# Optimization experiments

Measured on AMD Instinct MI355X. Metric: run time of the kernel, lower is better.

## Reference

```python
import jax, jax.numpy as jnp
import numpy as np

B, N, E1, H, D = 16, 256, 4, 8, 128  # batch, max nodes, edge types+1, heads, dim
VOCAB = 100


def setup_inputs() -> dict:
    key = jax.random.key(0)
    ks = jax.random.split(key, 20)
    s = 0.05
    return dict(
        node_feat=jax.random.randint(ks[0], (B, N), 0, VOCAB),
        L=jax.random.normal(ks[1], (B, N, N, E1), jnp.float32),
        emb=jax.random.normal(ks[2], (VOCAB, D), jnp.float32) * s,
        W0=jax.random.normal(ks[3], (E1, H, D, D), jnp.float32) * s,
        W1=jax.random.normal(ks[4], (E1, H, D * H * E1, D), jnp.float32) * (s / 4.0),
        a1w0=jax.random.normal(ks[5], (E1, H, D), jnp.float32) * s,
        a1b0=jnp.zeros((E1, H), jnp.float32),
        a2w0=jax.random.normal(ks[6], (E1, H, D), jnp.float32) * s,
        a2b0=jnp.zeros((E1, H), jnp.float32),
        a1w1=jax.random.normal(ks[7], (E1, H, D), jnp.float32) * s,
        a1b1=jnp.zeros((E1, H), jnp.float32),
        a2w1=jax.random.normal(ks[8], (E1, H, D), jnp.float32) * s,
        a2b1=jnp.zeros((E1, H), jnp.float32),
        sb0=jnp.zeros((E1, H, D), jnp.float32),
        sb1=jnp.zeros((E1, H, D), jnp.float32),
        outW=jax.random.normal(ks[9], (D, D), jnp.float32) * s,
        outb=jnp.zeros((D,), jnp.float32),
        attW=jax.random.normal(ks[10], (D,), jnp.float32) * s,
        attb=jnp.zeros((), jnp.float32),
    )


def _gat_layer(state, Ltr, W, a1w, a1b, a2w, a2b, sb, last):
    # state: (B, N, Din); W: (E1, H, Din, D); Ltr: (E1, 1, B, N, N)
    Wh = jnp.einsum('bni,ehio->ehbno', state, W)                      # (E1,H,B,N,D)
    s1 = jnp.einsum('ehbno,eho->ehbn', Wh, a1w) + a1b[:, :, None, None]
    s2 = jnp.einsum('ehbno,eho->ehbn', Wh, a2w) + a2b[:, :, None, None]
    logits = jax.nn.leaky_relu(s1[..., :, None] + s2[..., None, :], 0.2) + Ltr
    att = jax.nn.softmax(logits, axis=3)  # torch softmax over dim=1 of (B,N,N)
    h = jnp.einsum('ehbnm,ehbmo->ehbno', att, Wh) + sb[:, :, None, None, :]
    if last:
        return jnp.mean(h, axis=(0, 1))                               # (B,N,D)
    h = jax.nn.elu(h)
    # concat order in torch: outer edge-type jj, inner head ii -> (B,N,E1*H*D)
    return jnp.transpose(h, (2, 3, 0, 1, 4)).reshape(state.shape[0], state.shape[1], -1)


def reference(node_feat, L, emb, W0, W1, a1w0, a1b0, a2w0, a2b0,
              a1w1, a1b1, a2w1, a2b1, sb0, sb1, outW, outb, attW, attb):
    Ltr = jnp.transpose(L, (3, 0, 1, 2))[:, None]  # (E1,1,B,N,N)
    state = emb[node_feat]                         # (B,N,D)
    state = _gat_layer(state, Ltr, W0, a1w0, a1b0, a2w0, a2b0, sb0, last=False)
    state = _gat_layer(state, Ltr, W1, a1w1, a1b1, a2w1, a2b1, sb1, last=True)
    y = state @ outW + outb                        # (B,N,D)
    aw = jax.nn.sigmoid(state @ attW + attb)       # (B,N)
    y = aw[..., None] * y
    return jnp.mean(y, axis=1)                     # (B,D)
```

## Files before the change

kernel.cpp:

```cpp
#include <hip/hip_runtime.h>
#include <hip/hip_bf16.h>

#define Bq 16
#define Nq 256
#define E1q 4
#define Hq 8
#define Dq 128
#define EH 32
#define BN 4096

typedef __hip_bfloat16 bf16;
typedef short bf16x8 __attribute__((ext_vector_type(8)));
typedef float f32x4 __attribute__((ext_vector_type(4)));

__device__ __forceinline__ void gll16(const void* gptr, void* lptr) {
    __builtin_amdgcn_global_load_lds(
        (const __attribute__((address_space(1))) void*)gptr,
        (__attribute__((address_space(3))) void*)lptr, 16, 0, 0);
}

__device__ __forceinline__ unsigned short f2bf(float v) {
    __hip_bfloat16 h = __float2bfloat16(v);
    return *(unsigned short*)&h;
}

__device__ __forceinline__ void transpose_tile(const float* __restrict__ W,
                                               bf16* __restrict__ WT, int K,
                                               int kt, int nt, int eh,
                                               float (*tile)[65], int tid) {
    int tr = tid >> 6, tc = tid & 63;
    const float* src = W + ((size_t)eh * K + kt * 64) * 128 + nt * 64;
#pragma unroll
    for (int p = 0; p < 16; ++p) {
        int r = p * 4 + tr;
        tile[r][tc] = src[(size_t)r * 128 + tc];
    }
    __syncthreads();
    bf16* dst = WT + ((size_t)eh * 128 + nt * 64) * K + kt * 64;
    int cg = tid & 15, rs = tid >> 4;
#pragma unroll
    for (int p = 0; p < 4; ++p) {
        int n = rs + 16 * p;
        ushort4 pk;
        pk.x = f2bf(tile[cg * 4 + 0][n]);
        pk.y = f2bf(tile[cg * 4 + 1][n]);
        pk.z = f2bf(tile[cg * 4 + 2][n]);
        pk.w = f2bf(tile[cg * 4 + 3][n]);
        *(ushort4*)(dst + (size_t)n * K + cg * 4) = pk;
    }
}

__global__ __launch_bounds__(256) void prep_kernel(const int* __restrict__ nf,
                                                   const float* __restrict__ emb,
                                                   const float* __restrict__ W0,
                                                   const float* __restrict__ W1,
                                                   const float* __restrict__ L,
                                                   bf16* __restrict__ st0b,
                                                   bf16* __restrict__ W0T,
                                                   bf16* __restrict__ W1T,
                                                   float* __restrict__ Le) {
    int bid = blockIdx.x;
    int t = threadIdx.x;
    __shared__ float tile[64][65];
    if (bid < 2048) {
        int i = bid * 256 + t;
        int row = i >> 7, col = i & 127;
        st0b[i] = __float2bfloat16(emb[nf[row] * Dq + col]);
    } else if (bid < 2176) {
        int id2 = bid - 2048;
        transpose_tile(W0, W0T, 128, id2 & 1, (id2 >> 1) & 1, id2 >> 2, tile, t);
    } else if (bid < 6272) {
        int id3 = bid - 2176;
        transpose_tile(W1, W1T, 4096, id3 & 63, (id3 >> 6) & 1, id3 >> 7, tile, t);
    } else {
        int idx = (bid - 6272) * 256 + t;
        float4 v = *(const float4*)(L + (size_t)idx * 4);
        Le[idx] = v.x;
        Le[1048576 + idx] = v.y;
        Le[2097152 + idx] = v.z;
        Le[3145728 + idx] = v.w;
    }
}

__global__ __launch_bounds__(256) void mfma_gemm_kernel(const bf16* __restrict__ Ab,
                                                        const bf16* __restrict__ Bt,
                                                        bf16* __restrict__ Wht,
                                                        const float* __restrict__ a1w,
                                                        const float* __restrict__ a1b,
                                                        const float* __restrict__ a2w,
                                                        const float* __restrict__ a2b,
                                                        float* __restrict__ s1,
                                                        float* __restrict__ s2, int K) {
    int id = blockIdx.x;
    int xcd = id & 7, slot = id >> 3;
    int eh = (slot & 3) * 8 + xcd;
    int rt = slot >> 2;
    int tid = threadIdx.x;
    int w = tid >> 6, l = tid & 63;
    int q = l >> 4, mn = l & 15;
    __shared__ __align__(16) bf16 As[128 * 64];
    __shared__ __align__(16) bf16 Bs[128 * 64];
    __shared__ float red1[128], red2[128];
    const bf16* Ap = Ab + (size_t)(rt * 128) * K;
    const bf16* Bp = Bt + (size_t)eh * 128 * K;
    int lr = l >> 3;
    int g = (l & 7) ^ lr;
    int gcol = g * 8;

    if (tid < 128) { red1[tid] = 0.f; red2[tid] = 0.f; }

    f32x4 acc[4][4];
#pragma unroll
    for (int i = 0; i < 4; i++)
#pragma unroll
        for (int j = 0; j < 4; j++) acc[i][j] = (f32x4){0.f, 0.f, 0.f, 0.f};

    int wr = (w >> 1) * 64, wc = (w & 1) * 64;
    int msw = mn & 7;

    for (int k0 = 0; k0 < K; k0 += 64) {
#pragma unroll
        for (int u = 0; u < 4; ++u) {
            int i = w * 4 + u;
            int r = i * 8 + lr;
            gll16(Ap + (size_t)r * K + k0 + gcol, (char*)As + i * 1024);
            gll16(Bp + (size_t)r * K + k0 + gcol, (char*)Bs + i * 1024);
        }
        __syncthreads();
#pragma unroll
        for (int kk = 0; kk < 2; ++kk) {
            int qb = ((kk * 4 + q) ^ msw) * 16;
            bf16x8 af[4], bfr[4];
#pragma unroll
            for (int i = 0; i < 4; ++i) {
                af[i]  = *(const bf16x8*)((const char*)As + (wr + i * 16 + mn) * 128 + qb);
                bfr[i] = *(const bf16x8*)((const char*)Bs + (wc + i * 16 + mn) * 128 + qb);
            }
#pragma unroll
            for (int i = 0; i < 4; ++i)
#pragma unroll
                for (int j = 0; j < 4; ++j)
                    acc[i][j] = __builtin_amdgcn_mfma_f32_16x16x32_bf16(af[i], bfr[j], acc[i][j], 0, 0, 0);
        }
        __syncthreads();
    }
#pragma unroll
    for (int i = 0; i < 4; ++i) {
        int r0 = rt * 128 + wr + i * 16 + q * 4;
        int b = r0 >> 8, m = r0 & 255;
#pragma unroll
        for (int j = 0; j < 4; ++j) {
            int o = wc + j * 16 + mn;
            ushort4 pk;
            pk.x = f2bf(acc[i][j][0]);
            pk.y = f2bf(acc[i][j][1]);
            pk.z = f2bf(acc[i][j][2]);
            pk.w = f2bf(acc[i][j][3]);
            *(ushort4*)(Wht + ((((size_t)eh * 16 + b) * 128 + o) * 256 + m)) = pk;
        }
    }
    float w1v[4], w2v[4];
#pragma unroll
    for (int j = 0; j < 4; ++j) {
        int o = wc + j * 16 + mn;
        w1v[j] = a1w[eh * 128 + o];
        w2v[j] = a2w[eh * 128 + o];
    }
#pragma unroll
    for (int i = 0; i < 4; ++i)
#pragma unroll
        for (int r = 0; r < 4; ++r) {
            float p1 = 0.f, p2 = 0.f;
#pragma unroll
            for (int j = 0; j < 4; ++j) {
                p1 += acc[i][j][r] * w1v[j];
                p2 += acc[i][j][r] * w2v[j];
            }
#pragma unroll
            for (int off = 1; off < 16; off <<= 1) {
                p1 += __shfl_xor(p1, off);
                p2 += __shfl_xor(p2, off);
            }
            if (mn == 0) {
                int row = wr + i * 16 + q * 4 + r;
                atomicAdd(&red1[row], p1);
                atomicAdd(&red2[row], p2);
            }
        }
    __syncthreads();
    if (tid < 128) {
        int rg = rt * 128 + tid;
        s1[eh * 4096 + rg] = red1[tid] + a1b[eh];
        s2[eh * 4096 + rg] = red2[tid] + a2b[eh];
    }
}

__global__ __launch_bounds__(512, 2) void gemm4k_kernel(const bf16* __restrict__ Ab,
                                                        const bf16* __restrict__ Bt,
                                                        bf16* __restrict__ Wht,
                                                        const float* __restrict__ a1w,
                                                        const float* __restrict__ a1b,
                                                        const float* __restrict__ a2w,
                                                        const float* __restrict__ a2b,
                                                        float* __restrict__ s1,
                                                        float* __restrict__ s2) {
    __shared__ __align__(16) char smem[131072];
    int bid = blockIdx.x;
    int wg = (bid & 7) * 32 + (bid >> 3);
    int tm = wg >> 4, tn = wg & 15;
    int tid = threadIdx.x;
    int wid = tid >> 6, l = tid & 63;
    int wr = wid >> 2, wc = wid & 3;
    int lhi = l >> 4, llo = l & 15;
    int skq = (l & 7) ^ ((l >> 3) & 7);

    const bf16* Ap = Ab + (size_t)tm * 256 * 4096;
    const bf16* Bp = Bt + (size_t)tn * 256 * 4096;
    const bf16* sA = Ap + (size_t)(wid * 8 + (l >> 3)) * 4096 + skq * 8;
    const bf16* sB = Bp + (size_t)(wid * 8 + (l >> 3)) * 4096 + skq * 8;
    char* dA = (char*)smem + wid * 1024;
    char* dB = (char*)smem + 32768 + wid * 1024;

    auto stA = [&](int tt, int s) {
        gll16(sA + (size_t)s * 64 * 4096 + tt * 64, dA + (tt & 1) * 65536 + s * 8192);
    };
    auto stB = [&](int tt, int s) {
        gll16(sB + (size_t)s * 64 * 4096 + tt * 64, dB + (tt & 1) * 65536 + s * 8192);
    };

    f32x4 acc[8][4];
#pragma unroll
    for (int i = 0; i < 8; ++i)
#pragma unroll
        for (int j = 0; j < 4; ++j) acc[i][j] = (f32x4){0.f, 0.f, 0.f, 0.f};

    int kp0 = ((lhi)     ^ (llo & 7)) << 4;
    int kp1 = ((4 + lhi) ^ (llo & 7)) << 4;
    int aoff = (wr * 64 + llo) << 7;
    int boff = 32768 + ((wc * 32 + llo) << 7);

    stA(0, 0); stA(0, 1); stB(0, 0); stB(0, 1);
    stA(0, 2); stA(0, 3); stB(0, 2); stB(0, 3);
    asm volatile("s_waitcnt vmcnt(0)" ::: "memory");
    __builtin_amdgcn_s_barrier();
    bf16x8 A0[4][2], A1[4][2], B0[2][2], B1[2][2];
    {
        const char* sm0 = (const char*)smem;
#pragma unroll
        for (int m = 0; m < 4; ++m) {
            A0[m][0] = *(const bf16x8*)(sm0 + aoff + m * 2048 + kp0);
            A0[m][1] = *(const bf16x8*)(sm0 + aoff + m * 2048 + kp1);
        }
#pragma unroll
        for (int n = 0; n < 2; ++n) {
            B0[n][0] = *(const bf16x8*)(sm0 + boff + n * 2048 + kp0);
            B0[n][1] = *(const bf16x8*)(sm0 + boff + n * 2048 + kp1);
        }
    }

#pragma unroll 1
    for (int t = 0; t < 64; ++t) {
        const char* smc = (const char*)smem + (t & 1) * 65536;
        const char* smn = (const char*)smem + (((t + 1) & 1)) * 65536;
#pragma unroll
        for (int m = 0; m < 4; ++m) {
            A1[m][0] = *(const bf16x8*)(smc + aoff + 16384 + m * 2048 + kp0);
            A1[m][1] = *(const bf16x8*)(smc + aoff + 16384 + m * 2048 + kp1);
        }
        if (t < 63) { stA(t + 1, 0); stA(t + 1, 1); stB(t + 1, 0); stB(t + 1, 1); }
        asm volatile("s_waitcnt lgkmcnt(8)" ::: "memory");
        __builtin_amdgcn_sched_barrier(0);
        __builtin_amdgcn_s_setprio(1);
#pragma unroll
        for (int ks = 0; ks < 2; ++ks)
#pragma unroll
            for (int m = 0; m < 4; ++m)
#pragma unroll
                for (int n = 0; n < 2; ++n)
                    acc[m][n] = __builtin_amdgcn_mfma_f32_16x16x32_bf16(A0[m][ks], B0[n][ks], acc[m][n], 0, 0, 0);
        __builtin_amdgcn_s_setprio(0);
#pragma unroll
        for (int n = 0; n < 2; ++n) {
            B1[n][0] = *(const bf16x8*)(smc + boff + 16384 + n * 2048 + kp0);
            B1[n][1] = *(const bf16x8*)(smc + boff + 16384 + n * 2048 + kp1);
        }
        if (t < 63) { stA(t + 1, 2); stA(t + 1, 3); stB(t + 1, 2); stB(t + 1, 3); }
        asm volatile("s_waitcnt lgkmcnt(4)" ::: "memory");
        __builtin_amdgcn_sched_barrier(0);
        __builtin_amdgcn_s_setprio(1);
#pragma unroll
        for (int ks = 0; ks < 2; ++ks)
#pragma unroll
            for (int m = 0; m < 4; ++m)
#pragma unroll
                for (int n = 0; n < 2; ++n)
                    acc[4 + m][n] = __builtin_amdgcn_mfma_f32_16x16x32_bf16(A1[m][ks], B0[n][ks], acc[4 + m][n], 0, 0, 0);
        __builtin_amdgcn_s_setprio(0);
        asm volatile("s_waitcnt lgkmcnt(0)" ::: "memory");
        __builtin_amdgcn_sched_barrier(0);
        __builtin_amdgcn_s_setprio(1);
#pragma unroll
        for (int ks = 0; ks < 2; ++ks)
#pragma unroll
            for (int m = 0; m < 4; ++m)
#pragma unroll
                for (int n = 0; n < 2; ++n)
                    acc[m][2 + n] = __builtin_amdgcn_mfma_f32_16x16x32_bf16(A0[m][ks], B1[n][ks], acc[m][2 + n], 0, 0, 0);
        __builtin_amdgcn_s_setprio(0);
        if (t < 63) { asm volatile("s_waitcnt vmcnt(4)" ::: "memory"); }
        __builtin_amdgcn_s_barrier();
        if (t < 63) {
#pragma unroll
            for (int m = 0; m < 4; ++m) {
                A0[m][0] = *(const bf16x8*)(smn + aoff + m * 2048 + kp0);
                A0[m][1] = *(const bf16x8*)(smn + aoff + m * 2048 + kp1);
            }
#pragma unroll
            for (int n = 0; n < 2; ++n) {
                B0[n][0] = *(const bf16x8*)(smn + boff + n * 2048 + kp0);
                B0[n][1] = *(const bf16x8*)(smn + boff + n * 2048 + kp1);
            }
        }
        __builtin_amdgcn_sched_barrier(0);
        __builtin_amdgcn_s_setprio(1);
#pragma unroll
        for (int ks = 0; ks < 2; ++ks)
#pragma unroll
            for (int m = 0; m < 4; ++m)
#pragma unroll
                for (int n = 0; n < 2; ++n)
                    acc[4 + m][2 + n] = __builtin_amdgcn_mfma_f32_16x16x32_bf16(A1[m][ks], B1[n][ks], acc[4 + m][2 + n], 0, 0, 0);
        __builtin_amdgcn_s_setprio(0);
        if (t < 63) { asm volatile("s_waitcnt vmcnt(0)" ::: "memory"); }
        __builtin_amdgcn_s_barrier();
    }

    float* red = (float*)smem;
    red[tid] = 0.f;
    red[tid + 512] = 0.f;
    float w1v[4], w2v[4];
#pragma unroll
    for (int n = 0; n < 4; ++n) {
        int eh = tn * 2 + (n >> 1);
        int o = wc * 32 + (n & 1) * 16 + llo;
        w1v[n] = a1w[eh * 128 + o];
        w2v[n] = a2w[eh * 128 + o];
    }
    __syncthreads();
#pragma unroll
    for (int mi = 0; mi < 8; ++mi) {
        int R = (mi >> 2) * 128 + wr * 64 + (mi & 3) * 16 + lhi * 4;
#pragma unroll
        for (int n = 0; n < 4; ++n) {
            int eh = tn * 2 + (n >> 1);
            int o = wc * 32 + (n & 1) * 16 + llo;
            ushort4 pk;
            pk.x = f2bf(acc[mi][n][0]);
            pk.y = f2bf(acc[mi][n][1]);
            pk.z = f2bf(acc[mi][n][2]);
            pk.w = f2bf(acc[mi][n][3]);
            *(ushort4*)(Wht + ((((size_t)eh * 16 + tm) * 128 + o) * 256 + R)) = pk;
        }
#pragma unroll
        for (int r = 0; r < 4; ++r) {
            float p10 = acc[mi][0][r] * w1v[0] + acc[mi][1][r] * w1v[1];
            float p11 = acc[mi][2][r] * w1v[2] + acc[mi][3][r] * w1v[3];
            float p20 = acc[mi][0][r] * w2v[0] + acc[mi][1][r] * w2v[1];
            float p21 = acc[mi][2][r] * w2v[2] + acc[mi][3][r] * w2v[3];
#pragma unroll
            for (int off = 1; off < 16; off <<= 1) {
                p10 += __shfl_xor(p10, off);
                p11 += __shfl_xor(p11, off);
                p20 += __shfl_xor(p20, off);
                p21 += __shfl_xor(p21, off);
            }
            if (llo == 0) {
                int row = R + r;
                atomicAdd(&red[row], p10);
                atomicAdd(&red[256 + row], p11);
                atomicAdd(&red[512 + row], p20);
                atomicAdd(&red[768 + row], p21);
            }
        }
    }
    __syncthreads();
    {
        int ehl = tid >> 8, row = tid & 255;
        int eh = tn * 2 + ehl;
        s1[eh * 4096 + tm * 256 + row] = red[ehl * 256 + row] + a1b[eh];
        s2[eh * 4096 + tm * 256 + row] = red[512 + ehl * 256 + row] + a2b[eh];
    }
}

__global__ __launch_bounds__(256) void colsoft_kernel(const float* __restrict__ s1,
                                                      const float* __restrict__ s2,
                                                      const float* __restrict__ Le,
                                                      float4* __restrict__ stat) {
    int mt = blockIdx.x, b = blockIdx.y, e = blockIdx.z;
    int t = threadIdx.x;
    __shared__ float Lt[256 * 32];
    __shared__ float s1L[8 * 256];
#pragma unroll
    for (int i = 0; i < 8; ++i) s1L[i * 256 + t] = s1[(e * 8 + i) * 4096 + b * 256 + t];
    const float* Lb = Le + ((size_t)(e * 16 + b) * 256) * 256 + mt * 32;
#pragma unroll
    for (int j = 0; j < 8; ++j) {
        int f = t + 256 * j;
        int n = f >> 3, c4 = (f & 7) * 4;
        *(float4*)(Lt + n * 32 + c4) = *(const float4*)(Lb + (size_t)n * 256 + c4);
    }
    __syncthreads();
    int h = t >> 5, mm = t & 31;
    int m = mt * 32 + mm;
    float s2v = s2[(e * 8 + h) * 4096 + b * 256 + m];
    const float* s1p = s1L + h * 256;
    float s1max = -1e30f;
#pragma unroll
    for (int u = 0; u < 8; ++u) s1max = fmaxf(s1max, s1p[mm * 8 + u]);
#pragma unroll
    for (int off = 16; off; off >>= 1) s1max = fmaxf(s1max, __shfl_xor(s1max, off));
    float sm = s1max + s2v;
    float bound = (sm > 0.f ? sm : 0.2f * sm) + 8.0f;
    float sum = 0.f;
    for (int n = 0; n < 256; ++n) {
        float x = s1p[n] + s2v;
        x = x > 0.f ? x : 0.2f * x;
        x += Lt[n * 32 + mm];
        sum += __expf(x - bound);
    }
    float4 st = {s2v, bound, 1.0f / sum, 0.f};
    stat[(e * 8 + h) * 4096 + b * 256 + m] = st;
}

template <int LAST>
__global__ __launch_bounds__(256) void att_mfma_kernel(const float* __restrict__ s1,
                                                       const float4* __restrict__ stat,
                                                       const float* __restrict__ Le,
                                                       const bf16* __restrict__ Wht,
                                                       const float* __restrict__ sb,
                                                       bf16* __restrict__ outb) {
    int nt = blockIdx.x;
    int b = blockIdx.y;
    int eh = blockIdx.z;
    int e = eh >> 3;
    int tid = threadIdx.x;
    int w = tid >> 6, l = tid & 63;
    int q = l >> 4, mn = l & 15;
    __shared__ __align__(16) bf16 As[128 * 32];
    __shared__ __align__(16) bf16 Bs[128 * 40];
    __shared__ float s1L[128];
    __shared__ __align__(16) float4 stL[256];

    int base = eh * 4096 + b * 256;
    if (tid < 128) s1L[tid] = s1[base + nt * 128 + tid];
    stL[tid] = stat[base + tid];
    __syncthreads();

    const bf16* Whtp = Wht + ((size_t)eh * 16 + b) * 32768;
    int nl = tid >> 1, mh = (tid & 1) * 16;
    const float* Lrow = Le + (((size_t)(e * 16 + b) * 256) + nt * 128 + nl) * 256;
    float s1v = s1L[nl];
    int srow = l >> 2;
    int sq = (l & 3) ^ ((l >> 3) & 3);
    int scol = sq * 8;
    int rsw = ((mn >> 1) & 3) << 3;

    f32x4 acc[4][4];
#pragma unroll
    for (int i = 0; i < 4; i++)
#pragma unroll
        for (int j = 0; j < 4; j++) acc[i][j] = (f32x4){0.f, 0.f, 0.f, 0.f};

    int wr = (w >> 1) * 64, wc = (w & 1) * 64;

    float4 lv[4];
#pragma unroll
    for (int jj = 0; jj < 4; ++jj) lv[jj] = *(const float4*)(Lrow + mh + jj * 4);

    for (int k0 = 0; k0 < 256; k0 += 32) {
#pragma unroll
        for (int u = 0; u < 2; ++u) {
            int i = 2 * w + u;
            gll16(Whtp + (size_t)(i * 16 + srow) * 256 + k0 + scol, (char*)As + i * 1024);
        }
        float4 cur[4];
#pragma unroll
        for (int jj = 0; jj < 4; ++jj) cur[jj] = lv[jj];
        if (k0 + 32 < 256) {
#pragma unroll
            for (int jj = 0; jj < 4; ++jj)
                lv[jj] = *(const float4*)(Lrow + k0 + 32 + mh + jj * 4);
        }
#pragma unroll
        for (int jj = 0; jj < 4; ++jj) {
            int mb = mh + jj * 4;
            float av[4];
#pragma unroll
            for (int c = 0; c < 4; ++c) {
                int m = k0 + mb + c;
                float4 stv = stL[m];
                float x = s1v + stv.x;
                x = x > 0.f ? x : 0.2f * x;
                x += ((const float*)&cur[jj])[c];
                av[c] = __expf(x - stv.y) * stv.z;
            }
            unsigned int u01 = (unsigned int)f2bf(av[0]) | ((unsigned int)f2bf(av[1]) << 16);
            unsigned int u23 = (unsigned int)f2bf(av[2]) | ((unsigned int)f2bf(av[3]) << 16);
            unsigned int* bp = (unsigned int*)Bs + (nl * 40 + mb) / 2;
            bp[0] = u01;
            bp[1] = u23;
        }
        __syncthreads();
        bf16x8 af[4], bfr[4];
#pragma unroll
        for (int i = 0; i < 4; ++i) {
            af[i]  = *(const bf16x8*)(As + (wr + i * 16 + mn) * 32 + ((q << 3) ^ rsw));
            bfr[i] = *(const bf16x8*)(Bs + (wc + i * 16 + mn) * 40 + q * 8);
        }
#pragma unroll
        for (int i = 0; i < 4; ++i)
#pragma unroll
            for (int j = 0; j < 4; ++j)
                acc[i][j] = __builtin_amdgcn_mfma_f32_16x16x32_bf16(af[i], bfr[j], acc[i][j], 0, 0, 0);
        __syncthreads();
    }
#pragma unroll
    for (int i = 0; i < 4; ++i) {
        int o0 = wr + i * 16 + q * 4;
        float4 sbv = *(const float4*)(sb + eh * 128 + o0);
#pragma unroll
        for (int j = 0; j < 4; ++j) {
            int n = wc + j * 16 + mn;
            float v0 = acc[i][j][0] + sbv.x;
            float v1 = acc[i][j][1] + sbv.y;
            float v2 = acc[i][j][2] + sbv.z;
            float v3 = acc[i][j][3] + sbv.w;
            if (LAST == 0) {
                v0 = v0 > 0.f ? v0 : __expf(v0) - 1.f;
                v1 = v1 > 0.f ? v1 : __expf(v1) - 1.f;
                v2 = v2 > 0.f ? v2 : __expf(v2) - 1.f;
                v3 = v3 > 0.f ? v3 : __expf(v3) - 1.f;
                ushort4 pk = {f2bf(v0), f2bf(v1), f2bf(v2), f2bf(v3)};
                *(ushort4*)(outb + (size_t)(b * 256 + nt * 128 + n) * 4096 + eh * Dq + o0) = pk;
            } else {
                ushort4 pk = {f2bf(v0), f2bf(v1), f2bf(v2), f2bf(v3)};
                *(ushort4*)(outb + ((size_t)eh * 4096 + b * 256 + nt * 128 + n) * Dq + o0) = pk;
            }
        }
    }
}

__global__ __launch_bounds__(256) void reduce_aw_kernel(const bf16* __restrict__ h2b,
                                                        const float* __restrict__ attW,
                                                        const float* __restrict__ attb,
                                                        float* __restrict__ st2,
                                                        float* __restrict__ aw) {
    int t = threadIdx.x;
    int rl = t >> 7, o = t & 127;
    int r = blockIdx.x * 2 + rl;
    float acc = 0.f;
#pragma unroll
    for (int eh = 0; eh < EH; ++eh)
        acc += __bfloat162float(h2b[((size_t)eh * 4096 + r) * 128 + o]);
    acc *= (1.0f / 32.0f);
    st2[(size_t)r * 128 + o] = acc;
    float p = acc * attW[o];
#pragma unroll
    for (int off = 32; off; off >>= 1) p += __shfl_down(p, off);
    __shared__ float part[4];
    if ((t & 63) == 0) part[t >> 6] = p;
    __syncthreads();
    if (t == 0) aw[r] = 1.0f / (1.0f + __expf(-(part[0] + part[1] + attb[0])));
    if (t == 128) aw[r] = 1.0f / (1.0f + __expf(-(part[2] + part[3] + attb[0])));
}

__global__ __launch_bounds__(128) void final_kernel(const float* __restrict__ st2,
                                                    const float* __restrict__ aw,
                                                    const float* __restrict__ outW,
                                                    const float* __restrict__ outb,
                                                    float* __restrict__ out) {
    int b = blockIdx.x;
    int t = threadIdx.x;
    __shared__ float awL[256], zL[128];
    awL[t] = aw[b * 256 + t];
    awL[t + 128] = aw[b * 256 + t + 128];
    __syncthreads();
    float z = 0.f;
    for (int n = 0; n < 256; ++n) z += awL[n] * st2[(size_t)(b * 256 + n) * Dq + t];
    float sa = 0.f;
    for (int n = 0; n < 256; ++n) sa += awL[n];
    zL[t] = z;
    __syncthreads();
    float acc = sa * outb[t];
    for (int o = 0; o < Dq; ++o) acc += zL[o] * outW[o * Dq + t];
    out[b * Dq + t] = acc * (1.0f / 256.0f);
}

extern "C" void kernel_launch(void* const* d_in, const int* in_sizes, int n_in,
                              void* d_out, int out_size, void* d_ws, size_t ws_size,
                              hipStream_t stream) {
    const int* nf = (const int*)d_in[0];
    const float* L = (const float*)d_in[1];
    const float* emb = (const float*)d_in[2];
    const float* W0 = (const float*)d_in[3];
    const float* W1 = (const float*)d_in[4];
    const float* a1w0 = (const float*)d_in[5];
    const float* a1b0 = (const float*)d_in[6];
    const float* a2w0 = (const float*)d_in[7];
    const float* a2b0 = (const float*)d_in[8];
    const float* a1w1 = (const float*)d_in[9];
    const float* a1b1 = (const float*)d_in[10];
    const float* a2w1 = (const float*)d_in[11];
    const float* a2b1 = (const float*)d_in[12];
    const float* sb0 = (const float*)d_in[13];
    const float* sb1 = (const float*)d_in[14];
    const float* outW = (const float*)d_in[15];
    const float* outb = (const float*)d_in[16];
    const float* attW = (const float*)d_in[17];
    const float* attb = (const float*)d_in[18];

    char* p = (char*)d_ws;
    bf16* st0b = (bf16*)(p);
    bf16* W0T  = (bf16*)(p + 1048576);
    bf16* W1T  = (bf16*)(p + 2097152);
    bf16* st1b = (bf16*)(p + 35651584);
    bf16* h2b  = (bf16*)(p + 2097152);
    float* Le  = (float*)(p + 69206016);
    bf16* Wht  = (bf16*)(p + 85983232);
    float* s1  = (float*)(p + 119537664);
    float* s2  = (float*)(p + 120061952);
    float4* stat = (float4*)(p + 120586240);
    float* st2 = (float*)(p);
    float* aw  = s1;
    float* outp = (float*)d_out;

    prep_kernel<<<10368, 256, 0, stream>>>(nf, emb, W0, W1, L, st0b, W0T, W1T, Le);

    mfma_gemm_kernel<<<1024, 256, 0, stream>>>(st0b, W0T, Wht, a1w0, a1b0, a2w0, a2b0, s1, s2, 128);
    colsoft_kernel<<<dim3(8, 16, 4), 256, 0, stream>>>(s1, s2, Le, stat);
    att_mfma_kernel<0><<<dim3(2, 16, 32), 256, 0, stream>>>(s1, stat, Le, Wht, sb0, st1b);

    gemm4k_kernel<<<256, 512, 0, stream>>>(st1b, W1T, Wht, a1w1, a1b1, a2w1, a2b1, s1, s2);
    colsoft_kernel<<<dim3(8, 16, 4), 256, 0, stream>>>(s1, s2, Le, stat);
    att_mfma_kernel<1><<<dim3(2, 16, 32), 256, 0, stream>>>(s1, stat, Le, Wht, sb1, h2b);

    reduce_aw_kernel<<<2048, 256, 0, stream>>>(h2b, attW, attb, st2, aw);
    final_kernel<<<16, 128, 0, stream>>>(st2, aw, outW, outb, outp);
}
```

Measured before the change: 412.4 us.

## Load GEMM B operand directly from global into registers, halving LDS

The B tiles of the 4K GEMM are no longer staged through LDS. Each wave now reads its B fragments straight from global memory into registers, fetching the next k-step at the end of each iteration. Only A stays double-buffered in LDS, so LDS drops from 128KB to 64KB and one barrier per iteration goes away, which could let two workgroups share a CU. The cost is that waves with different wr values fetch the same B data twice. The per-lane global loads are also strided and poorly coalesced, and their latency sits right before the next iteration's MFMAs, which may stall.

```diff
diff --git a/kernel.cpp b/kernel.cpp
--- a/kernel.cpp
+++ b/kernel.cpp
@@ -204,7 +204,7 @@
                                                         const float* __restrict__ a2b,
                                                         float* __restrict__ s1,
                                                         float* __restrict__ s2) {
-    __shared__ __align__(16) char smem[131072];
+    __shared__ __align__(16) char smem[65536];
     int bid = blockIdx.x;
     int wg = (bid & 7) * 32 + (bid >> 3);
     int tm = wg >> 4, tn = wg & 15;
@@ -217,16 +217,13 @@
     const bf16* Ap = Ab + (size_t)tm * 256 * 4096;
     const bf16* Bp = Bt + (size_t)tn * 256 * 4096;
     const bf16* sA = Ap + (size_t)(wid * 8 + (l >> 3)) * 4096 + skq * 8;
-    const bf16* sB = Bp + (size_t)(wid * 8 + (l >> 3)) * 4096 + skq * 8;
     char* dA = (char*)smem + wid * 1024;
-    char* dB = (char*)smem + 32768 + wid * 1024;
 
     auto stA = [&](int tt, int s) {
-        gll16(sA + (size_t)s * 64 * 4096 + tt * 64, dA + (tt & 1) * 65536 + s * 8192);
+        gll16(sA + (size_t)s * 64 * 4096 + tt * 64, dA + (tt & 1) * 32768 + s * 8192);
     };
-    auto stB = [&](int tt, int s) {
-        gll16(sB + (size_t)s * 64 * 4096 + tt * 64, dB + (tt & 1) * 65536 + s * 8192);
-    };
+
+    const bf16* bq = Bp + (size_t)(wc * 32 + llo) * 4096 + lhi * 8;
 
     f32x4 acc[8][4];
 #pragma unroll
@@ -237,13 +234,19 @@
     int kp0 = ((lhi)     ^ (llo & 7)) << 4;
     int kp1 = ((4 + lhi) ^ (llo & 7)) << 4;
     int aoff = (wr * 64 + llo) << 7;
-    int boff = 32768 + ((wc * 32 + llo) << 7);
-
-    stA(0, 0); stA(0, 1); stB(0, 0); stB(0, 1);
-    stA(0, 2); stA(0, 3); stB(0, 2); stB(0, 3);
-    asm volatile("s_waitcnt vmcnt(0)" ::: "memory");
+
+    bf16x8 A0[4][2], A1[4][2], B0[2][2], B1[2][2];
+
+    stA(0, 0); stA(0, 1); stA(0, 2); stA(0, 3);
+#pragma unroll
+    for (int n = 0; n < 2; ++n) {
+        B0[n][0] = *(const bf16x8*)(bq + (size_t)(n * 16) * 4096);
+        B0[n][1] = *(const bf16x8*)(bq + (size_t)(n * 16) * 4096 + 32);
+        B1[n][0] = *(const bf16x8*)(bq + (size_t)(128 + n * 16) * 4096);
+        B1[n][1] = *(const bf16x8*)(bq + (size_t)(128 + n * 16) * 4096 + 32);
+    }
+    asm volatile("s_waitcnt vmcnt(8)" ::: "memory");
     __builtin_amdgcn_s_barrier();
-    bf16x8 A0[4][2], A1[4][2], B0[2][2], B1[2][2];
     {
         const char* sm0 = (const char*)smem;
 #pragma unroll
@@ -251,23 +254,20 @@
             A0[m][0] = *(const bf16x8*)(sm0 + aoff + m * 2048 + kp0);
             A0[m][1] = *(const bf16x8*)(sm0 + aoff + m * 2048 + kp1);
         }
-#pragma unroll
-        for (int n = 0; n < 2; ++n) {
-            B0[n][0] = *(const bf16x8*)(sm0 + boff + n * 2048 + kp0);
-            B0[n][1] = *(const bf16x8*)(sm0 + boff + n * 2048 + kp1);
-        }
     }
 
 #pragma unroll 1
     for (int t = 0; t < 64; ++t) {
-        const char* smc = (const char*)smem + (t & 1) * 65536;
-        const char* smn = (const char*)smem + (((t + 1) & 1)) * 65536;
+        const char* smc = (const char*)smem + (t & 1) * 32768;
+        const char* smn = (const char*)smem + (((t + 1) & 1)) * 32768;
 #pragma unroll
         for (int m = 0; m < 4; ++m) {
             A1[m][0] = *(const bf16x8*)(smc + aoff + 16384 + m * 2048 + kp0);
             A1[m][1] = *(const bf16x8*)(smc + aoff + 16384 + m * 2048 + kp1);
         }
-        if (t < 63) { stA(t + 1, 0); stA(t + 1, 1); stB(t + 1, 0); stB(t + 1, 1); }
+        if (t < 63) { stA(t + 1, 0); stA(t + 1, 1); stA(t + 1, 2); stA(t + 1, 3); }
+        if (t < 63) { asm volatile("s_waitcnt vmcnt(8)" ::: "memory"); }
+        else        { asm volatile("s_waitcnt vmcnt(4)" ::: "memory"); }
         asm volatile("s_waitcnt lgkmcnt(8)" ::: "memory");
         __builtin_amdgcn_sched_barrier(0);
         __builtin_amdgcn_s_setprio(1);
@@ -278,23 +278,6 @@
 #pragma unroll
                 for (int n = 0; n < 2; ++n)
                     acc[m][n] = __builtin_amdgcn_mfma_f32_16x16x32_bf16(A0[m][ks], B0[n][ks], acc[m][n], 0, 0, 0);
-        __builtin_amdgcn_s_setprio(0);
-#pragma unroll
-        for (int n = 0; n < 2; ++n) {
-            B1[n][0] = *(const bf16x8*)(smc + boff + 16384 + n * 2048 + kp0);
-            B1[n][1] = *(const bf16x8*)(smc + boff + 16384 + n * 2048 + kp1);
-        }
-        if (t < 63) { stA(t + 1, 2); stA(t + 1, 3); stB(t + 1, 2); stB(t + 1, 3); }
-        asm volatile("s_waitcnt lgkmcnt(4)" ::: "memory");
-        __builtin_amdgcn_sched_barrier(0);
-        __builtin_amdgcn_s_setprio(1);
-#pragma unroll
-        for (int ks = 0; ks < 2; ++ks)
-#pragma unroll
-            for (int m = 0; m < 4; ++m)
-#pragma unroll
-                for (int n = 0; n < 2; ++n)
-                    acc[4 + m][n] = __builtin_amdgcn_mfma_f32_16x16x32_bf16(A1[m][ks], B0[n][ks], acc[4 + m][n], 0, 0, 0);
         __builtin_amdgcn_s_setprio(0);
         asm volatile("s_waitcnt lgkmcnt(0)" ::: "memory");
         __builtin_amdgcn_sched_barrier(0);
@@ -305,9 +288,21 @@
             for (int m = 0; m < 4; ++m)
 #pragma unroll
                 for (int n = 0; n < 2; ++n)
+                    acc[4 + m][n] = __builtin_amdgcn_mfma_f32_16x16x32_bf16(A1[m][ks], B0[n][ks], acc[4 + m][n], 0, 0, 0);
+        __builtin_amdgcn_s_setprio(0);
+        if (t < 63) { asm volatile("s_waitcnt vmcnt(4)" ::: "memory"); }
+        else        { asm volatile("s_waitcnt vmcnt(0)" ::: "memory"); }
+        __builtin_amdgcn_sched_barrier(0);
+        __builtin_amdgcn_s_setprio(1);
+#pragma unroll
+        for (int ks = 0; ks < 2; ++ks)
+#pragma unroll
+            for (int m = 0; m < 4; ++m)
+#pragma unroll
+                for (int n = 0; n < 2; ++n)
                     acc[m][2 + n] = __builtin_amdgcn_mfma_f32_16x16x32_bf16(A0[m][ks], B1[n][ks], acc[m][2 + n], 0, 0, 0);
         __builtin_amdgcn_s_setprio(0);
-        if (t < 63) { asm volatile("s_waitcnt vmcnt(4)" ::: "memory"); }
+        if (t < 63) { asm volatile("s_waitcnt vmcnt(0)" ::: "memory"); }
         __builtin_amdgcn_s_barrier();
         if (t < 63) {
 #pragma unroll
@@ -315,11 +310,6 @@
                 A0[m][0] = *(const bf16x8*)(smn + aoff + m * 2048 + kp0);
                 A0[m][1] = *(const bf16x8*)(smn + aoff + m * 2048 + kp1);
             }
-#pragma unroll
-            for (int n = 0; n < 2; ++n) {
-                B0[n][0] = *(const bf16x8*)(smn + boff + n * 2048 + kp0);
-                B0[n][1] = *(const bf16x8*)(smn + boff + n * 2048 + kp1);
-            }
         }
         __builtin_amdgcn_sched_barrier(0);
         __builtin_amdgcn_s_setprio(1);
@@ -331,8 +321,16 @@
                 for (int n = 0; n < 2; ++n)
                     acc[4 + m][2 + n] = __builtin_amdgcn_mfma_f32_16x16x32_bf16(A1[m][ks], B1[n][ks], acc[4 + m][2 + n], 0, 0, 0);
         __builtin_amdgcn_s_setprio(0);
-        if (t < 63) { asm volatile("s_waitcnt vmcnt(0)" ::: "memory"); }
-        __builtin_amdgcn_s_barrier();
+        if (t < 63) {
+            int kb = (t + 1) * 64;
+#pragma unroll
+            for (int n = 0; n < 2; ++n) {
+                B0[n][0] = *(const bf16x8*)(bq + (size_t)(n * 16) * 4096 + kb);
+                B0[n][1] = *(const bf16x8*)(bq + (size_t)(n * 16) * 4096 + kb + 32);
+                B1[n][0] = *(const bf16x8*)(bq + (size_t)(128 + n * 16) * 4096 + kb);
+                B1[n][1] = *(const bf16x8*)(bq + (size_t)(128 + n * 16) * 4096 + kb + 32);
+            }
+        }
     }
 
     float* red = (float*)smem;
```

New measurement: 498.2 us. 1.21x slower.
